# Optimization experiments

Hardware: AMD Instinct MI355X
Metric: run time of the kernel (lower is better)

## Reference

```python
import jax, jax.numpy as jnp
import numpy as np

B, S, V, E, H, OOV = 64, 512, 50257, 512, 1024, 12


def setup_inputs() -> dict:
    key = jax.random.key(0)
    ks = jax.random.split(key, 16)
    s = 0.02
    return {
        "input_idx": jax.random.randint(ks[0], (B,), 0, V),
        "encoded": jax.random.normal(ks[1], (B, S, 2 * H), dtype=jnp.float32),
        "encoded_idx": jax.random.randint(ks[2], (B, S), 0, V),
        "prev_state": jax.random.normal(ks[3], (B, H), dtype=jnp.float32),
        "weighted": jax.random.normal(ks[4], (B, 1, 2 * H), dtype=jnp.float32),
        "order": 1,
        "embed": jax.random.normal(ks[5], (V, E), dtype=jnp.float32) * s,
        "gru_wi": jax.random.normal(ks[6], (3 * H, E + 2 * H), dtype=jnp.float32) * s,
        "gru_wh": jax.random.normal(ks[7], (3 * H, H), dtype=jnp.float32) * s,
        "gru_bi": jnp.zeros((3 * H,), dtype=jnp.float32),
        "gru_bh": jnp.zeros((3 * H,), dtype=jnp.float32),
        "Ws_w": jax.random.normal(ks[8], (H, 2 * H), dtype=jnp.float32) * s,
        "Ws_b": jnp.zeros((H,), dtype=jnp.float32),
        "Wg_w": jax.random.normal(ks[9], (V, H), dtype=jnp.float32) * s,
        "Wg_b": jnp.zeros((V,), dtype=jnp.float32),
        "Wc_w": jax.random.normal(ks[10], (H, 2 * H), dtype=jnp.float32) * s,
        "Wc_b": jnp.zeros((H,), dtype=jnp.float32),
    }


def reference(input_idx, encoded, encoded_idx, prev_state, weighted, order,
              embed, gru_wi, gru_wh, gru_bi, gru_bh, Ws_w, Ws_b,
              Wg_w, Wg_b, Wc_w, Wc_b):
    if order == 0:  # static Python branch, matches the torch init branch
        prev_state = encoded[:, -1] @ Ws_w.T + Ws_b
        weighted = jnp.zeros((encoded.shape[0], 1, 2 * H), dtype=encoded.dtype)

    # one-step GRU (torch GRU gate order: r, z, n)
    x = jnp.concatenate([embed[input_idx], weighted[:, 0]], axis=-1)  # [B, E+2H]
    gi = x @ gru_wi.T + gru_bi
    gh = prev_state @ gru_wh.T + gru_bh
    gi_r, gi_z, gi_n = jnp.split(gi, 3, axis=-1)
    gh_r, gh_z, gh_n = jnp.split(gh, 3, axis=-1)
    r = jax.nn.sigmoid(gi_r + gh_r)
    z = jax.nn.sigmoid(gi_z + gh_z)
    n = jnp.tanh(gi_n + r * gh_n)
    state = (1.0 - z) * n + z * prev_state  # [B, H]

    # generate scores over vocab
    score_g = state @ Wg_w.T + Wg_b  # [B, V]

    # copy scores over source positions
    sc = jnp.tanh(jnp.einsum('bsd,hd->bsh', encoded, Wc_w) + Wc_b)  # [B, S, H]
    score_c = jnp.tanh(jnp.einsum('bsh,bh->bs', sc, state))
    score_c = score_c + jnp.where(encoded_idx == 0, -1000.0, 0.0)

    # joint softmax over generate + copy
    probs = jax.nn.softmax(jnp.concatenate([score_g, score_c], axis=1), axis=1)
    prob_g = probs[:, :V]
    prob_c = probs[:, V:]  # [B, S]

    # extend with OOV slots (+1e-4 as in torch code)
    prob_g = jnp.concatenate(
        [prob_g, jnp.full((prob_g.shape[0], OOV), 1e-4, dtype=prob_g.dtype)], axis=1)

    # prob_c -> vocab: scatter-add by source token id (== one-hot bmm in torch)
    def scatter_row(p, idx):
        return jnp.zeros((V + OOV,), dtype=p.dtype).at[idx].add(p)
    prob_c_to_g = jax.vmap(scatter_row)(prob_c, encoded_idx)  # [B, V+OOV]

    out = (prob_g + prob_c_to_g)[:, None, :]  # [B, 1, V+OOV]

    # attention restricted to source positions equal to input token, normalized
    m = (encoded_idx == input_idx[:, None]).astype(encoded.dtype)  # [B, S]
    ssum = m.sum(axis=1, keepdims=True)
    m = jnp.where(ssum > 1, m / jnp.maximum(ssum, 1.0), m)
    attn = prob_c * m
    weighted_out = jnp.einsum('bs,bsd->bd', attn, encoded)[:, None, :]  # [B, 1, 2H]

    return out, state, weighted_out
```

## Files before the change

kernel.cpp:

```cpp
#include <hip/hip_runtime.h>

#define B_    64
#define S_    512
#define V_    50257
#define E_    512
#define H_    1024
#define OOV_  12
#define VO_   (V_ + OOV_)
#define NTOT_ (V_ + S_)

typedef float  f32x4  __attribute__((ext_vector_type(4)));
typedef __bf16 bf16x8 __attribute__((ext_vector_type(8)));
typedef unsigned short ushort8 __attribute__((ext_vector_type(8)));

__device__ __forceinline__ unsigned short f2bf(float f) {
  union { float f; unsigned u; } c; c.f = f;
  unsigned r = c.u + 0x7FFFu + ((c.u >> 16) & 1u);
  return (unsigned short)(r >> 16);
}
__device__ __forceinline__ ushort8 cvt8(float4 u0, float4 u1) {
  ushort8 p;
  p[0] = f2bf(u0.x); p[1] = f2bf(u0.y); p[2] = f2bf(u0.z); p[3] = f2bf(u0.w);
  p[4] = f2bf(u1.x); p[5] = f2bf(u1.y); p[6] = f2bf(u1.z); p[7] = f2bf(u1.w);
  return p;
}

__global__ __launch_bounds__(256)
void cvt_bf16(const float* __restrict__ in, unsigned short* __restrict__ out, int n8)
{
  int i = blockIdx.x * 256 + threadIdx.x;
  const int stride = gridDim.x * 256;
  for (; i < n8; i += stride) {
    float4 u0 = ((const float4*)in)[2 * i];
    float4 u1 = ((const float4*)in)[2 * i + 1];
    ((ushort8*)out)[i] = cvt8(u0, u1);
  }
}

__global__ __launch_bounds__(256)
void build_x(const int* __restrict__ idx, const float* __restrict__ embed,
             const float* __restrict__ weighted, unsigned short* __restrict__ xb)
{
  const int t = blockIdx.x * 256 + threadIdx.x;
  if (t >= B_ * 320) return;
  const int m = t / 320, k = (t % 320) * 8;
  const float* src = (k < E_) ? &embed[(size_t)idx[m] * E_ + k]
                              : &weighted[(size_t)m * (2 * H_) + (k - E_)];
  float4 u0 = *(const float4*)src;
  float4 u1 = *(const float4*)(src + 4);
  ((ushort8*)xb)[t] = cvt8(u0, u1);
}

#define TILE 128
#define BK   64

template<int MODE, int ACVT, int BCVT>
__global__ __launch_bounds__(256)
void gemm_bf(const unsigned short* __restrict__ Ab, const float* __restrict__ Af,
             const unsigned short* __restrict__ Bb, const float* __restrict__ Bf,
             const float* __restrict__ bias, const float* __restrict__ statev,
             float* __restrict__ out, int M, int N, int K, int ntn)
{
  __shared__ unsigned short lds_a[TILE * BK];
  __shared__ unsigned short lds_b[TILE * BK];
  __shared__ float rowsum[TILE];

  const int tid  = threadIdx.x;
  const int bid  = blockIdx.x;
  const int m0 = (bid / ntn) * TILE, n0 = (bid % ntn) * TILE;

  const int lane = tid & 63;
  const int wave = tid >> 6;
  const int wrow = wave >> 1, wcol = wave & 1;
  const int lm   = lane & 15, quad = lane >> 4;

  f32x4 acc[4][4];
  #pragma unroll
  for (int i = 0; i < 4; ++i)
    #pragma unroll
    for (int j = 0; j < 4; ++j) { f32x4 z = {0.f, 0.f, 0.f, 0.f}; acc[i][j] = z; }

  for (int kt = 0; kt < K; kt += BK) {
    if (ACVT) {
      const int r = tid >> 1;
      const int grow = min(m0 + r, M - 1);
      const float* __restrict__ base = &Af[(size_t)grow * K + kt];
      #pragma unroll
      for (int q = 0; q < 4; ++q) {
        const int j = (tid & 1) * 4 + q;
        float4 u0 = *(const float4*)(base + j * 8);
        float4 u1 = *(const float4*)(base + j * 8 + 4);
        *(ushort8*)&lds_a[r * BK + (j ^ (r & 7)) * 8] = cvt8(u0, u1);
      }
    } else {
      #pragma unroll
      for (int t = 0; t < 4; ++t) {
        const int r  = (wave * 4 + t) * 8 + (lane >> 3);
        const int jg = (lane & 7) ^ (r & 7);
        const int grow = min(m0 + r, M - 1);
        const unsigned short* g = &Ab[(size_t)grow * K + kt + jg * 8];
        __builtin_amdgcn_global_load_lds(
            (const __attribute__((address_space(1))) void*)g,
            (__attribute__((address_space(3))) void*)&lds_a[(wave * 4 + t) * 512],
            16, 0, 0);
      }
    }
    if (BCVT) {
      const int r = tid >> 1;
      const int grow = min(n0 + r, N - 1);
      const float* __restrict__ base = &Bf[(size_t)grow * K + kt];
      #pragma unroll
      for (int q = 0; q < 4; ++q) {
        const int j = (tid & 1) * 4 + q;
        float4 u0 = *(const float4*)(base + j * 8);
        float4 u1 = *(const float4*)(base + j * 8 + 4);
        *(ushort8*)&lds_b[r * BK + (j ^ (r & 7)) * 8] = cvt8(u0, u1);
      }
    } else {
      #pragma unroll
      for (int t = 0; t < 4; ++t) {
        const int r  = (wave * 4 + t) * 8 + (lane >> 3);
        const int jg = (lane & 7) ^ (r & 7);
        const int grow = min(n0 + r, N - 1);
        const unsigned short* g = &Bb[(size_t)grow * K + kt + jg * 8];
        __builtin_amdgcn_global_load_lds(
            (const __attribute__((address_space(1))) void*)g,
            (__attribute__((address_space(3))) void*)&lds_b[(wave * 4 + t) * 512],
            16, 0, 0);
      }
    }
    __syncthreads();

    #pragma unroll
    for (int ks = 0; ks < BK; ks += 32) {
      const int c0 = ks >> 3;
      bf16x8 av[4], bv[4];
      #pragma unroll
      for (int i = 0; i < 4; ++i) {
        const int r = wrow * 64 + i * 16 + lm;
        av[i] = *(const bf16x8*)&lds_a[r * BK + (((c0 + quad) ^ (lm & 7)) * 8)];
      }
      #pragma unroll
      for (int j = 0; j < 4; ++j) {
        const int r = wcol * 64 + j * 16 + lm;
        bv[j] = *(const bf16x8*)&lds_b[r * BK + (((c0 + quad) ^ (lm & 7)) * 8)];
      }
      #pragma unroll
      for (int i = 0; i < 4; ++i)
        #pragma unroll
        for (int j = 0; j < 4; ++j)
          acc[i][j] = __builtin_amdgcn_mfma_f32_16x16x32_bf16(av[i], bv[j], acc[i][j], 0, 0, 0);
    }
    __syncthreads();
  }

  if (MODE == 0) {
    #pragma unroll
    for (int i = 0; i < 4; ++i) {
      const int rbase = m0 + wrow * 64 + i * 16 + quad * 4;
      #pragma unroll
      for (int j = 0; j < 4; ++j) {
        const int col = n0 + wcol * 64 + j * 16 + lm;
        if (col < N) {
          const float bv2 = bias[col];
          #pragma unroll
          for (int r = 0; r < 4; ++r) {
            const int row = rbase + r;
            if (row < M) out[(size_t)row * N + col] = acc[i][j][r] + bv2;
          }
        }
      }
    }
  } else {
    if (tid < TILE) rowsum[tid] = 0.f;
    __syncthreads();
    #pragma unroll
    for (int i = 0; i < 4; ++i) {
      #pragma unroll
      for (int r = 0; r < 4; ++r) {
        const int rloc = wrow * 64 + i * 16 + quad * 4 + r;
        const int row  = m0 + rloc;
        const int b    = row >> 9;
        float p = 0.f;
        #pragma unroll
        for (int j = 0; j < 4; ++j) {
          const int col = wcol * 64 + j * 16 + lm;
          const float v = acc[i][j][r] + bias[col];
          p += tanhf(v) * statev[b * H_ + col];
        }
        p += __shfl_xor(p, 1);
        p += __shfl_xor(p, 2);
        p += __shfl_xor(p, 4);
        p += __shfl_xor(p, 8);
        if (lm == 0) atomicAdd(&rowsum[rloc], p);
      }
    }
    __syncthreads();
    if (tid < TILE) atomicAdd(&out[m0 + tid], rowsum[tid]);
  }
}

__global__ __launch_bounds__(256)
void gru_combine(const float* __restrict__ gis, const float* __restrict__ ghs,
                 const float* __restrict__ prev, float* __restrict__ state,
                 unsigned short* __restrict__ st_bf)
{
  const int idx = blockIdx.x * 256 + threadIdx.x;
  const int b = idx >> 10, h = idx & (H_ - 1);
  const float* gib = gis + (size_t)b * 3 * H_;
  const float* ghb = ghs + (size_t)b * 3 * H_;
  const float r = 1.f / (1.f + expf(-(gib[h]      + ghb[h])));
  const float z = 1.f / (1.f + expf(-(gib[H_ + h] + ghb[H_ + h])));
  const float n = tanhf(gib[2 * H_ + h] + r * ghb[2 * H_ + h]);
  const float s = (1.f - z) * n + z * prev[idx];
  state[idx] = s;
  st_bf[idx] = f2bf(s);
}

#define CH  2048
#define NCH 25

__global__ __launch_bounds__(256)
void softmax_chunk(const float* __restrict__ score_g, const float* __restrict__ acc_c,
                   const int* __restrict__ eidx, float* __restrict__ mc, float* __restrict__ lc)
{
  const int b = blockIdx.y, c = blockIdx.x, tid = threadIdx.x;
  const int start = c * CH;
  const int end   = min(start + CH, NTOT_);
  __shared__ float red[4];

  float lmax = -1e30f;
  for (int i = start + tid; i < end; i += 256) {
    float v;
    if (i < V_) v = score_g[(size_t)b * V_ + i];
    else {
      const int s = i - V_;
      v = tanhf(acc_c[b * S_ + s]) + (eidx[b * S_ + s] == 0 ? -1000.f : 0.f);
    }
    lmax = fmaxf(lmax, v);
  }
  #pragma unroll
  for (int o = 32; o > 0; o >>= 1) lmax = fmaxf(lmax, __shfl_xor(lmax, o));
  if ((tid & 63) == 0) red[tid >> 6] = lmax;
  __syncthreads();
  lmax = fmaxf(fmaxf(red[0], red[1]), fmaxf(red[2], red[3]));
  __syncthreads();

  float lsum = 0.f;
  for (int i = start + tid; i < end; i += 256) {
    float v;
    if (i < V_) v = score_g[(size_t)b * V_ + i];
    else {
      const int s = i - V_;
      v = tanhf(acc_c[b * S_ + s]) + (eidx[b * S_ + s] == 0 ? -1000.f : 0.f);
    }
    lsum += expf(v - lmax);
  }
  #pragma unroll
  for (int o = 32; o > 0; o >>= 1) lsum += __shfl_xor(lsum, o);
  if ((tid & 63) == 0) red[tid >> 6] = lsum;
  __syncthreads();
  if (tid == 0) {
    mc[b * NCH + c] = lmax;
    lc[b * NCH + c] = red[0] + red[1] + red[2] + red[3];
  }
}

__global__ void softmax_combine(const float* __restrict__ mc, const float* __restrict__ lc,
                                float* __restrict__ Mrow, float* __restrict__ invL)
{
  const int b = threadIdx.x;
  float M = -1e30f;
  for (int c = 0; c < NCH; ++c) M = fmaxf(M, mc[b * NCH + c]);
  float L = 0.f;
  for (int c = 0; c < NCH; ++c) L += lc[b * NCH + c] * expf(mc[b * NCH + c] - M);
  Mrow[b] = M;
  invL[b] = 1.f / L;
}

__global__ __launch_bounds__(256)
void write_probg(const float* __restrict__ score_g, const float* __restrict__ Mrow,
                 const float* __restrict__ invL, float* __restrict__ out)
{
  const int b = blockIdx.y;
  const int v = blockIdx.x * 256 + threadIdx.x;
  if (v >= VO_) return;
  float val;
  if (v < V_) val = expf(score_g[(size_t)b * V_ + v] - Mrow[b]) * invL[b];
  else        val = 1e-4f;
  out[(size_t)b * VO_ + v] = val;
}

__global__ __launch_bounds__(256)
void scatter_weighted(const float* __restrict__ acc_c, const int* __restrict__ eidx,
                      const int* __restrict__ input_idx, const float* __restrict__ encoded,
                      const float* __restrict__ Mrow, const float* __restrict__ invL,
                      float* __restrict__ out, float* __restrict__ wout)
{
  __shared__ float pv[S_];
  __shared__ int   mlist[S_];
  __shared__ int   mcnt;
  const int b = blockIdx.x, tid = threadIdx.x;
  if (tid == 0) mcnt = 0;
  __syncthreads();

  const int   ii = input_idx[b];
  const float M  = Mrow[b], il = invL[b];
  for (int s = tid; s < S_; s += 256) {
    const int e = eidx[b * S_ + s];
    const float v = tanhf(acc_c[b * S_ + s]) + (e == 0 ? -1000.f : 0.f);
    const float p = expf(v - M) * il;
    pv[s] = p;
    atomicAdd(&out[(size_t)b * VO_ + e], p);
    if (e == ii) { const int pos = atomicAdd(&mcnt, 1); mlist[pos] = s; }
  }
  __syncthreads();

  const int cnt = mcnt;
  const float norm = cnt > 1 ? 1.f / (float)cnt : 1.f;
  for (int d = tid; d < 2 * H_; d += 256) {
    float a = 0.f;
    for (int t2 = 0; t2 < cnt; ++t2) {
      const int s = mlist[t2];
      a += pv[s] * encoded[((size_t)b * S_ + s) * (2 * H_) + d];
    }
    wout[(size_t)b * 2 * H_ + d] = a * norm;
  }
}

extern "C" void kernel_launch(void* const* d_in, const int* in_sizes, int n_in,
                              void* d_out, int out_size, void* d_ws, size_t ws_size,
                              hipStream_t stream)
{
  const int*   input_idx   = (const int*)  d_in[0];
  const float* encoded     = (const float*)d_in[1];
  const int*   encoded_idx = (const int*)  d_in[2];
  const float* prev_state  = (const float*)d_in[3];
  const float* weighted    = (const float*)d_in[4];
  const float* embed       = (const float*)d_in[6];
  const float* gru_wi      = (const float*)d_in[7];
  const float* gru_wh      = (const float*)d_in[8];
  const float* gru_bi      = (const float*)d_in[9];
  const float* gru_bh      = (const float*)d_in[10];
  const float* Wg_w        = (const float*)d_in[13];
  const float* Wg_b        = (const float*)d_in[14];
  const float* Wc_w        = (const float*)d_in[15];
  const float* Wc_b        = (const float*)d_in[16];

  float* out0  = (float*)d_out;
  float* state = out0 + (size_t)B_ * VO_;
  float* wout  = state + (size_t)B_ * H_;

  float* score_g = (float*)d_ws;
  float* gis     = score_g + (size_t)B_ * V_;
  float* ghs     = gis + (size_t)B_ * 3 * H_;
  float* acc_c   = ghs + (size_t)B_ * 3 * H_;
  float* mc      = acc_c + (size_t)B_ * S_;
  float* lc      = mc + B_ * NCH;
  float* Mrow    = lc + B_ * NCH;
  float* invL    = Mrow + B_;

  unsigned short* ub = (unsigned short*)(invL + B_);
  ub = (unsigned short*)(((uintptr_t)ub + 15) & ~(uintptr_t)15);
  unsigned short* x_bf  = ub;  ub += (size_t)B_ * (E_ + 2 * H_);
  unsigned short* ps_bf = ub;  ub += (size_t)B_ * H_;
  unsigned short* st_bf = ub;  ub += (size_t)B_ * H_;
  unsigned short* wc_bf = ub;
  unsigned short* wi_bf = wc_bf + (size_t)H_ * 2 * H_;
  unsigned short* wh_bf = wi_bf + (size_t)3 * H_ * (E_ + 2 * H_);
  unsigned short* end_small = wh_bf + (size_t)3 * H_ * H_;
  unsigned short* wg_bf  = end_small;
  unsigned short* end_wg = wg_bf + (size_t)V_ * H_;
  unsigned short* enc_bf = end_wg;
  unsigned short* end_enc = enc_bf + (size_t)B_ * S_ * 2 * H_;

  const bool cv_small = ws_size >= (size_t)((char*)end_small - (char*)d_ws);
  const bool cv_wg    = ws_size >= (size_t)((char*)end_wg    - (char*)d_ws);
  const bool cv_enc   = ws_size >= (size_t)((char*)end_enc   - (char*)d_ws);

  hipMemsetAsync(acc_c, 0, (size_t)B_ * S_ * sizeof(float), stream);

  dim3 blk(256);

  build_x<<<80, blk, 0, stream>>>(input_idx, embed, weighted, x_bf);
  cvt_bf16<<<32, blk, 0, stream>>>(prev_state, ps_bf, B_ * H_ / 8);
  if (cv_small) {
    cvt_bf16<<<1024, blk, 0, stream>>>(Wc_w, wc_bf, H_ * 2 * H_ / 8);
    cvt_bf16<<<3840, blk, 0, stream>>>(gru_wi, wi_bf, 3 * H_ * (E_ + 2 * H_) / 8);
    cvt_bf16<<<1536, blk, 0, stream>>>(gru_wh, wh_bf, 3 * H_ * H_ / 8);
  }
  if (cv_wg)  cvt_bf16<<<8192, blk, 0, stream>>>(Wg_w, wg_bf, V_ * H_ / 8);
  if (cv_enc) cvt_bf16<<<8192, blk, 0, stream>>>(encoded, enc_bf, B_ * S_ * 2 * H_ / 8);

  if (cv_small) {
    gemm_bf<0,0,0><<<24, blk, 0, stream>>>(x_bf, nullptr, wi_bf, nullptr,
                                           gru_bi, nullptr, gis, B_, 3 * H_, E_ + 2 * H_, 24);
    gemm_bf<0,0,0><<<24, blk, 0, stream>>>(ps_bf, nullptr, wh_bf, nullptr,
                                           gru_bh, nullptr, ghs, B_, 3 * H_, H_, 24);
  } else {
    gemm_bf<0,0,1><<<24, blk, 0, stream>>>(x_bf, nullptr, nullptr, gru_wi,
                                           gru_bi, nullptr, gis, B_, 3 * H_, E_ + 2 * H_, 24);
    gemm_bf<0,0,1><<<24, blk, 0, stream>>>(ps_bf, nullptr, nullptr, gru_wh,
                                           gru_bh, nullptr, ghs, B_, 3 * H_, H_, 24);
  }
  gru_combine<<<(B_ * H_) / 256, blk, 0, stream>>>(gis, ghs, prev_state, state, st_bf);

  if (cv_wg)
    gemm_bf<0,0,0><<<393, blk, 0, stream>>>(st_bf, nullptr, wg_bf, nullptr,
                                            Wg_b, nullptr, score_g, B_, V_, H_, 393);
  else
    gemm_bf<0,0,1><<<393, blk, 0, stream>>>(st_bf, nullptr, nullptr, Wg_w,
                                            Wg_b, nullptr, score_g, B_, V_, H_, 393);

  if (cv_enc && cv_small)
    gemm_bf<1,0,0><<<2048, blk, 0, stream>>>(enc_bf, nullptr, wc_bf, nullptr,
                                             Wc_b, state, acc_c, B_ * S_, H_, 2 * H_, 8);
  else if (cv_enc)
    gemm_bf<1,0,1><<<2048, blk, 0, stream>>>(enc_bf, nullptr, nullptr, Wc_w,
                                             Wc_b, state, acc_c, B_ * S_, H_, 2 * H_, 8);
  else if (cv_small)
    gemm_bf<1,1,0><<<2048, blk, 0, stream>>>(nullptr, encoded, wc_bf, nullptr,
                                             Wc_b, state, acc_c, B_ * S_, H_, 2 * H_, 8);
  else
    gemm_bf<1,1,1><<<2048, blk, 0, stream>>>(nullptr, encoded, nullptr, Wc_w,
                                             Wc_b, state, acc_c, B_ * S_, H_, 2 * H_, 8);

  softmax_chunk<<<dim3(NCH, B_), blk, 0, stream>>>(score_g, acc_c, encoded_idx, mc, lc);
  softmax_combine<<<1, B_, 0, stream>>>(mc, lc, Mrow, invL);
  write_probg<<<dim3((VO_ + 255) / 256, B_), blk, 0, stream>>>(score_g, Mrow, invL, out0);
  scatter_weighted<<<B_, blk, 0, stream>>>(acc_c, encoded_idx, input_idx, encoded,
                                           Mrow, invL, out0, wout);
}
```

Before: 970.5 us.

## Split-K the GRU GEMMs with atomics and XCD-swizzle the copy-score GEMM

The two small GRU GEMMs, which had only 24 blocks each, now use split-K across 8 grid slices and accumulate into zeroed outputs with atomicAdd. The bias add moves into gru_combine. The large encoded×Wc GEMM gets an XCD-aware block-to-tile mapping so that blocks sharing A rows land on the same XCD and reuse its L2. The aim is to fill the GPU on the GRU step and improve cache locality on the copy GEMM, at the cost of atomic traffic, an extra memset and nondeterministic summation order.

```diff
diff --git a/kernel.cpp b/kernel.cpp
--- a/kernel.cpp
+++ b/kernel.cpp
@@ -54,20 +54,28 @@
 #define TILE 128
 #define BK   64
 
-template<int MODE, int ACVT, int BCVT>
+template<int MODE, int ACVT, int BCVT, int XSWZ>
 __global__ __launch_bounds__(256)
 void gemm_bf(const unsigned short* __restrict__ Ab, const float* __restrict__ Af,
              const unsigned short* __restrict__ Bb, const float* __restrict__ Bf,
              const float* __restrict__ bias, const float* __restrict__ statev,
-             float* __restrict__ out, int M, int N, int K, int ntn)
+             float* __restrict__ out, int M, int N, int K, int ntn, int Kc)
 {
   __shared__ unsigned short lds_a[TILE * BK];
   __shared__ unsigned short lds_b[TILE * BK];
-  __shared__ float rowsum[TILE];
 
   const int tid  = threadIdx.x;
   const int bid  = blockIdx.x;
-  const int m0 = (bid / ntn) * TILE, n0 = (bid % ntn) * TILE;
+  int m0, n0;
+  if (XSWZ) {
+    const int cpx = gridDim.x >> 6;
+    const int xcd = bid & 7, s = bid >> 3;
+    m0 = (xcd * cpx + (s >> 3)) * TILE;
+    n0 = (s & 7) * TILE;
+  } else {
+    m0 = (bid / ntn) * TILE;
+    n0 = (bid % ntn) * TILE;
+  }
 
   const int lane = tid & 63;
   const int wave = tid >> 6;
@@ -80,7 +88,10 @@
     #pragma unroll
     for (int j = 0; j < 4; ++j) { f32x4 z = {0.f, 0.f, 0.f, 0.f}; acc[i][j] = z; }
 
-  for (int kt = 0; kt < K; kt += BK) {
+  const int k0   = blockIdx.y * Kc;
+  const int kend = min(k0 + Kc, K);
+
+  for (int kt = k0; kt < kend; kt += BK) {
     if (ACVT) {
       const int r = tid >> 1;
       const int grow = min(m0 + r, M - 1);
@@ -171,7 +182,8 @@
         }
       }
     }
-  } else {
+  } else if (MODE == 1) {
+    float* rowsum = (float*)lds_b;
     if (tid < TILE) rowsum[tid] = 0.f;
     __syncthreads();
     #pragma unroll
@@ -197,21 +209,44 @@
     }
     __syncthreads();
     if (tid < TILE) atomicAdd(&out[m0 + tid], rowsum[tid]);
+  } else {
+    #pragma unroll
+    for (int i = 0; i < 4; ++i) {
+      const int rbase = m0 + wrow * 64 + i * 16 + quad * 4;
+      #pragma unroll
+      for (int j = 0; j < 4; ++j) {
+        const int col = n0 + wcol * 64 + j * 16 + lm;
+        if (col < N) {
+          #pragma unroll
+          for (int r = 0; r < 4; ++r) {
+            const int row = rbase + r;
+            if (row < M) atomicAdd(&out[(size_t)row * N + col], acc[i][j][r]);
+          }
+        }
+      }
+    }
   }
 }
 
 __global__ __launch_bounds__(256)
 void gru_combine(const float* __restrict__ gis, const float* __restrict__ ghs,
                  const float* __restrict__ prev, float* __restrict__ state,
-                 unsigned short* __restrict__ st_bf)
+                 unsigned short* __restrict__ st_bf,
+                 const float* __restrict__ bi, const float* __restrict__ bh)
 {
   const int idx = blockIdx.x * 256 + threadIdx.x;
   const int b = idx >> 10, h = idx & (H_ - 1);
   const float* gib = gis + (size_t)b * 3 * H_;
   const float* ghb = ghs + (size_t)b * 3 * H_;
-  const float r = 1.f / (1.f + expf(-(gib[h]      + ghb[h])));
-  const float z = 1.f / (1.f + expf(-(gib[H_ + h] + ghb[H_ + h])));
-  const float n = tanhf(gib[2 * H_ + h] + r * ghb[2 * H_ + h]);
+  const float gr = gib[h]          + bi[h];
+  const float hr = ghb[h]          + bh[h];
+  const float gz = gib[H_ + h]     + bi[H_ + h];
+  const float hz = ghb[H_ + h]     + bh[H_ + h];
+  const float gn = gib[2 * H_ + h] + bi[2 * H_ + h];
+  const float hn = ghb[2 * H_ + h] + bh[2 * H_ + h];
+  const float r = 1.f / (1.f + expf(-(gr + hr)));
+  const float z = 1.f / (1.f + expf(-(gz + hz)));
+  const float n = tanhf(gn + r * hn);
   const float s = (1.f - z) * n + z * prev[idx];
   state[idx] = s;
   st_bf[idx] = f2bf(s);
@@ -379,6 +414,7 @@
   const bool cv_enc   = ws_size >= (size_t)((char*)end_enc   - (char*)d_ws);
 
   hipMemsetAsync(acc_c, 0, (size_t)B_ * S_ * sizeof(float), stream);
+  hipMemsetAsync(gis, 0, (size_t)2 * B_ * 3 * H_ * sizeof(float), stream);
 
   dim3 blk(256);
 
@@ -393,37 +429,38 @@
   if (cv_enc) cvt_bf16<<<8192, blk, 0, stream>>>(encoded, enc_bf, B_ * S_ * 2 * H_ / 8);
 
   if (cv_small) {
-    gemm_bf<0,0,0><<<24, blk, 0, stream>>>(x_bf, nullptr, wi_bf, nullptr,
-                                           gru_bi, nullptr, gis, B_, 3 * H_, E_ + 2 * H_, 24);
-    gemm_bf<0,0,0><<<24, blk, 0, stream>>>(ps_bf, nullptr, wh_bf, nullptr,
-                                           gru_bh, nullptr, ghs, B_, 3 * H_, H_, 24);
+    gemm_bf<2,0,0,0><<<dim3(24, 8), blk, 0, stream>>>(x_bf, nullptr, wi_bf, nullptr,
+                                           nullptr, nullptr, gis, B_, 3 * H_, E_ + 2 * H_, 24, 320);
+    gemm_bf<2,0,0,0><<<dim3(24, 8), blk, 0, stream>>>(ps_bf, nullptr, wh_bf, nullptr,
+                                           nullptr, nullptr, ghs, B_, 3 * H_, H_, 24, 128);
   } else {
-    gemm_bf<0,0,1><<<24, blk, 0, stream>>>(x_bf, nullptr, nullptr, gru_wi,
-                                           gru_bi, nullptr, gis, B_, 3 * H_, E_ + 2 * H_, 24);
-    gemm_bf<0,0,1><<<24, blk, 0, stream>>>(ps_bf, nullptr, nullptr, gru_wh,
-                                           gru_bh, nullptr, ghs, B_, 3 * H_, H_, 24);
-  }
-  gru_combine<<<(B_ * H_) / 256, blk, 0, stream>>>(gis, ghs, prev_state, state, st_bf);
+    gemm_bf<2,0,1,0><<<dim3(24, 8), blk, 0, stream>>>(x_bf, nullptr, nullptr, gru_wi,
+                                           nullptr, nullptr, gis, B_, 3 * H_, E_ + 2 * H_, 24, 320);
+    gemm_bf<2,0,1,0><<<dim3(24, 8), blk, 0, stream>>>(ps_bf, nullptr, nullptr, gru_wh,
+                                           nullptr, nullptr, ghs, B_, 3 * H_, H_, 24, 128);
+  }
+  gru_combine<<<(B_ * H_) / 256, blk, 0, stream>>>(gis, ghs, prev_state, state, st_bf,
+                                                   gru_bi, gru_bh);
 
   if (cv_wg)
-    gemm_bf<0,0,0><<<393, blk, 0, stream>>>(st_bf, nullptr, wg_bf, nullptr,
-                                            Wg_b, nullptr, score_g, B_, V_, H_, 393);
+    gemm_bf<0,0,0,0><<<393, blk, 0, stream>>>(st_bf, nullptr, wg_bf, nullptr,
+                                            Wg_b, nullptr, score_g, B_, V_, H_, 393, H_);
   else
-    gemm_bf<0,0,1><<<393, blk, 0, stream>>>(st_bf, nullptr, nullptr, Wg_w,
-                                            Wg_b, nullptr, score_g, B_, V_, H_, 393);
+    gemm_bf<0,0,1,0><<<393, blk, 0, stream>>>(st_bf, nullptr, nullptr, Wg_w,
+                                            Wg_b, nullptr, score_g, B_, V_, H_, 393, H_);
 
   if (cv_enc && cv_small)
-    gemm_bf<1,0,0><<<2048, blk, 0, stream>>>(enc_bf, nullptr, wc_bf, nullptr,
-                                             Wc_b, state, acc_c, B_ * S_, H_, 2 * H_, 8);
+    gemm_bf<1,0,0,1><<<2048, blk, 0, stream>>>(enc_bf, nullptr, wc_bf, nullptr,
+                                             Wc_b, state, acc_c, B_ * S_, H_, 2 * H_, 8, 2 * H_);
   else if (cv_enc)
-    gemm_bf<1,0,1><<<2048, blk, 0, stream>>>(enc_bf, nullptr, nullptr, Wc_w,
-                                             Wc_b, state, acc_c, B_ * S_, H_, 2 * H_, 8);
+    gemm_bf<1,0,1,1><<<2048, blk, 0, stream>>>(enc_bf, nullptr, nullptr, Wc_w,
+                                             Wc_b, state, acc_c, B_ * S_, H_, 2 * H_, 8, 2 * H_);
   else if (cv_small)
-    gemm_bf<1,1,0><<<2048, blk, 0, stream>>>(nullptr, encoded, wc_bf, nullptr,
-                                             Wc_b, state, acc_c, B_ * S_, H_, 2 * H_, 8);
+    gemm_bf<1,1,0,1><<<2048, blk, 0, stream>>>(nullptr, encoded, wc_bf, nullptr,
+                                             Wc_b, state, acc_c, B_ * S_, H_, 2 * H_, 8, 2 * H_);
   else
-    gemm_bf<1,1,1><<<2048, blk, 0, stream>>>(nullptr, encoded, nullptr, Wc_w,
-                                             Wc_b, state, acc_c, B_ * S_, H_, 2 * H_, 8);
+    gemm_bf<1,1,1,1><<<2048, blk, 0, stream>>>(nullptr, encoded, nullptr, Wc_w,
+                                             Wc_b, state, acc_c, B_ * S_, H_, 2 * H_, 8, 2 * H_);
 
   softmax_chunk<<<dim3(NCH, B_), blk, 0, stream>>>(score_g, acc_c, encoded_idx, mc, lc);
   softmax_combine<<<1, B_, 0, stream>>>(mc, lc, Mrow, invL);
```

Result: faster. 893.2 us (-8.0%).
